# Kernel tuning notes

Hardware: AMD Instinct MI355X
Metric: run time of the kernel (lower is better)

Reference implementation:

```python
import jax, jax.numpy as jnp
import numpy as np
from jax import lax

B, N_SITES, FEAT, BOND, OUT = 2048, 128, 64, 32, 256
CORE_SCALE = 0.02  # keeps the 128-step matrix product finite


def setup_inputs() -> dict:
    key = jax.random.key(0)
    ks = jax.random.split(key, 6)
    return {
        "x": jax.random.normal(ks[0], (B, N_SITES, FEAT), dtype=jnp.float32),
        "cores": jax.random.normal(ks[1], (N_SITES, BOND, FEAT, BOND), dtype=jnp.float32) * CORE_SCALE,
        "start": jax.random.normal(ks[2], (1, BOND), dtype=jnp.float32),
        "end": jax.random.normal(ks[3], (BOND, 1), dtype=jnp.float32),
        "fc_w": jax.random.normal(ks[4], (OUT, 1), dtype=jnp.float32),
        "fc_b": jax.random.normal(ks[5], (OUT,), dtype=jnp.float32),
    }


def reference(x, cores, start, end, fc_w, fc_b):
    # x: [B, N, F]; cores: [N, D, F, D]; start: [1, D]; end: [D, 1]
    b = x.shape[0]
    res0 = jnp.broadcast_to(start, (b, start.shape[1]))  # [B, D]

    def step(res, site):
        xi, core = site  # xi: [B, F], core: [D, F, D]
        m = jnp.einsum('bf,dfr->bdr', xi, core)  # per-site transfer matrix [B, D, D]
        return jnp.einsum('bd,bdr->br', res, m), None

    res, _ = lax.scan(step, res0, (jnp.swapaxes(x, 0, 1), cores))
    val = res @ end  # [B, 1]
    return val @ fc_w.T + fc_b  # [B, OUT]
```

## Files before the change

kernel.cpp:

```cpp
#include <hip/hip_runtime.h>


#define NSITES 128
#define FEATD  64
#define BOND   32
#define OUTD   256
#define BT     16
#define SEGLEN 16
#define NSEG   (NSITES / SEGLEN)
#define NPAIR  (SEGLEN / 2)
#define NBT    (2048 / BT)

#define RSTRIDE 36
#define BSTRIDE 1164

typedef __attribute__((ext_vector_type(4))) float float4v;

__device__ __forceinline__ unsigned pk4_fp8(float a, float b, float c, float d) {
    int v = __builtin_amdgcn_cvt_pk_fp8_f32(a, b, 0, false);
    v = __builtin_amdgcn_cvt_pk_fp8_f32(c, d, v, true);
    return (unsigned)v;
}

__device__ __forceinline__ long ld8(const unsigned char* p) {
    unsigned lo = *(const unsigned*)p;
    unsigned hi = *(const unsigned*)(p + 4);
    return (long)(((unsigned long long)hi << 32) | (unsigned long long)lo);
}

__device__ __forceinline__ void af_load(long af[16], const unsigned char* __restrict__ core8,
                                        int n, int wave, int cl, int q) {
    const unsigned char* base = core8 + (size_t)n * (1024 * FEATD);
#pragma unroll
    for (int i = 0; i < 8; ++i) {
        const unsigned char* p = base + (size_t)((wave * 8 + i) * 16 + cl) * FEATD + q * 8;
        af[2 * i + 0] = *(const long*)p;
        af[2 * i + 1] = *(const long*)(p + 32);
    }
}

__device__ __forceinline__ long cvt_frag(float4v c0, float4v c1,
                                         int idxlo, int idxhi, int selhi) {
    const float s = 0.0625f;
    int d0 = (int)pk4_fp8(c0[0] * s, c0[1] * s, c0[2] * s, c0[3] * s);
    int d1 = (int)pk4_fp8(c1[0] * s, c1[1] * s, c1[2] * s, c1[3] * s);
    int l0 = __builtin_amdgcn_ds_bpermute(idxlo, d0);
    int l1 = __builtin_amdgcn_ds_bpermute(idxlo, d1);
    int h0 = __builtin_amdgcn_ds_bpermute(idxhi, d0);
    int h1 = __builtin_amdgcn_ds_bpermute(idxhi, d1);
    unsigned lo = (unsigned)(selhi ? l1 : l0);
    unsigned hi = (unsigned)(selhi ? h1 : h0);
    return (long)(((unsigned long long)hi << 32) | (unsigned long long)lo);
}

__global__ __launch_bounds__(256)
void prep_cores8(const float* __restrict__ cores, unsigned char* __restrict__ core8) {
    __shared__ float tile[FEATD][BOND + 4];
    const int nd = blockIdx.x;
    const int t  = threadIdx.x;
    const float* src = cores + (size_t)nd * (FEATD * BOND);
    {
        int base = t * 8;
        int f = base >> 5, r0 = base & 31;
        float4 v0 = *(const float4*)(src + base);
        float4 v1 = *(const float4*)(src + base + 4);
        tile[f][r0 + 0] = v0.x; tile[f][r0 + 1] = v0.y;
        tile[f][r0 + 2] = v0.z; tile[f][r0 + 3] = v0.w;
        tile[f][r0 + 4] = v1.x; tile[f][r0 + 5] = v1.y;
        tile[f][r0 + 6] = v1.z; tile[f][r0 + 7] = v1.w;
    }
    __syncthreads();
    const int r = t >> 3, f0 = (t & 7) * 8;
    const float s = 16.0f;
    unsigned lo = pk4_fp8(tile[f0 + 0][r] * s, tile[f0 + 1][r] * s,
                          tile[f0 + 2][r] * s, tile[f0 + 3][r] * s);
    unsigned hi = pk4_fp8(tile[f0 + 4][r] * s, tile[f0 + 5][r] * s,
                          tile[f0 + 6][r] * s, tile[f0 + 7][r] * s);
    uint2 w; w.x = lo; w.y = hi;
    *(uint2*)(core8 + ((size_t)nd * BOND + r) * FEATD + f0) = w;
}

__global__ __launch_bounds__(512, 4)
void mps_seg(const float* __restrict__ x, const unsigned char* __restrict__ core8,
             unsigned char* __restrict__ Pout) {
    __shared__ __align__(16) unsigned char MA[BT * BSTRIDE];
    __shared__ __align__(16) unsigned char MB[BT * BSTRIDE];
    __shared__ __align__(16) unsigned char XS[2][2][BT * 72];

    const int t    = threadIdx.x;
    const int wave = t >> 6;
    const int lane = t & 63;
    const int cl   = lane & 15;
    const int q    = lane >> 4;
    const int seg  = blockIdx.x;
    const int bt   = blockIdx.y;
    const int b0   = bt * BT;
    const int xb   = t >> 5, xf = (t & 31) * 2;

    const int idxlo = (cl + 16 * ((2 * q) & 3)) << 2;
    const int idxhi = (cl + 16 * ((2 * q + 1) & 3)) << 2;
    const int selhi = q >> 1;

    long ps[2][2];
#pragma unroll
    for (int J = 0; J < 2; ++J) {
        int row = J * 16 + cl;
        int jj  = row - 8 * q;
        long v  = (jj >= 0 && jj < 8) ? (long)(0x58ULL << (8 * jj)) : 0L;
        ps[0][J] = v;
        ps[1][J] = v;
    }

    const int n0 = seg * SEGLEN;

    const float* xptr = x + ((size_t)(b0 + xb) * NSITES + n0) * FEATD + xf;
    float2 xa  = *(const float2*)xptr;
    float2 xbv = *(const float2*)(xptr + FEATD);
    {
        int v0 = __builtin_amdgcn_cvt_pk_fp8_f32(xa.x, xa.y, 0, false);
        *(unsigned short*)&XS[0][0][xb * 72 + xf] = (unsigned short)(v0 & 0xffff);
        int v1 = __builtin_amdgcn_cvt_pk_fp8_f32(xbv.x, xbv.y, 0, false);
        *(unsigned short*)&XS[0][1][xb * 72 + xf] = (unsigned short)(v1 & 0xffff);
    }
    long afa[16];
    af_load(afa, core8, n0, wave, cl, q);
    __syncthreads();

    for (int j = 0; j < NPAIR; ++j) {
        const int n = n0 + 2 * j;

        {
            const unsigned char* xsA = &XS[j & 1][0][0];
            const unsigned char* xsB = &XS[j & 1][1][0];
            long bxa0 = *(const long*)(xsA + cl * 72 + q * 8);
            long bxa1 = *(const long*)(xsA + cl * 72 + 32 + q * 8);
            long bxb0 = *(const long*)(xsB + cl * 72 + q * 8);
            long bxb1 = *(const long*)(xsB + cl * 72 + 32 + q * 8);

            long afb[16];
            af_load(afb, core8, n + 1, wave, cl, q);

            float4v acc[8];
            __builtin_amdgcn_s_setprio(1);
#pragma unroll
            for (int i = 0; i < 8; ++i) {
                float4v z = {0.f, 0.f, 0.f, 0.f};
                z = __builtin_amdgcn_mfma_f32_16x16x32_fp8_fp8(afa[2 * i + 0], bxa0, z, 0, 0, 0);
                acc[i] = __builtin_amdgcn_mfma_f32_16x16x32_fp8_fp8(afa[2 * i + 1], bxa1, z, 0, 0, 0);
            }
            __builtin_amdgcn_s_setprio(0);
#pragma unroll
            for (int i = 0; i < 8; ++i) {
                unsigned w = pk4_fp8(acc[i][0], acc[i][1], acc[i][2], acc[i][3]);
                *(unsigned*)&MA[cl * BSTRIDE + (wave * 4 + (i >> 1)) * RSTRIDE
                                + (i & 1) * 16 + q * 4] = w;
            }

            if (j + 1 < NPAIR) {
                const float* xp = x + ((size_t)(b0 + xb) * NSITES + n + 2) * FEATD + xf;
                xa  = *(const float2*)xp;
                xbv = *(const float2*)(xp + FEATD);
            }

            float4v accb[8];
            __builtin_amdgcn_s_setprio(1);
#pragma unroll
            for (int i = 0; i < 8; ++i) {
                float4v z = {0.f, 0.f, 0.f, 0.f};
                z = __builtin_amdgcn_mfma_f32_16x16x32_fp8_fp8(afb[2 * i + 0], bxb0, z, 0, 0, 0);
                accb[i] = __builtin_amdgcn_mfma_f32_16x16x32_fp8_fp8(afb[2 * i + 1], bxb1, z, 0, 0, 0);
            }
            __builtin_amdgcn_s_setprio(0);
#pragma unroll
            for (int p = 0; p < 2; ++p)
#pragma unroll
                for (int g = 0; g < 4; ++g) {
                    unsigned w = pk4_fp8(accb[0 + p][g], accb[2 + p][g],
                                         accb[4 + p][g], accb[6 + p][g]);
                    *(unsigned*)&MB[cl * BSTRIDE + (16 * p + 4 * q + g) * RSTRIDE
                                    + wave * 4] = w;
                }
        }
        __syncthreads();

        {
            if (j + 1 < NPAIR) {
                int v0 = __builtin_amdgcn_cvt_pk_fp8_f32(xa.x, xa.y, 0, false);
                *(unsigned short*)&XS[(j + 1) & 1][0][xb * 72 + xf] = (unsigned short)(v0 & 0xffff);
                int v1 = __builtin_amdgcn_cvt_pk_fp8_f32(xbv.x, xbv.y, 0, false);
                *(unsigned short*)&XS[(j + 1) & 1][1][xb * 72 + xf] = (unsigned short)(v1 & 0xffff);
                af_load(afa, core8, n + 2, wave, cl, q);
            }

#pragma unroll
            for (int bi = 0; bi < 2; ++bi) {
                const int bb = wave * 2 + bi;
                const unsigned char* mab = &MA[bb * BSTRIDE];
                const unsigned char* mbb = &MB[bb * BSTRIDE];
                long pa0 = ld8(mab + cl * RSTRIDE + q * 8);
                long pa1 = ld8(mab + (16 + cl) * RSTRIDE + q * 8);
                long pb0 = ld8(mbb + cl * RSTRIDE + q * 8);
                long pb1 = ld8(mbb + (16 + cl) * RSTRIDE + q * 8);
                float4v z00 = {0.f, 0.f, 0.f, 0.f}, z01 = {0.f, 0.f, 0.f, 0.f};
                float4v z10 = {0.f, 0.f, 0.f, 0.f}, z11 = {0.f, 0.f, 0.f, 0.f};
                z00 = __builtin_amdgcn_mfma_f32_16x16x32_fp8_fp8(pa0, pb0, z00, 0, 0, 0);
                z01 = __builtin_amdgcn_mfma_f32_16x16x32_fp8_fp8(pa0, pb1, z01, 0, 0, 0);
                z10 = __builtin_amdgcn_mfma_f32_16x16x32_fp8_fp8(pa1, pb0, z10, 0, 0, 0);
                z11 = __builtin_amdgcn_mfma_f32_16x16x32_fp8_fp8(pa1, pb1, z11, 0, 0, 0);
                long ca0 = cvt_frag(z00, z10, idxlo, idxhi, selhi);
                long ca1 = cvt_frag(z01, z11, idxlo, idxhi, selhi);
                float4v c00 = {0.f, 0.f, 0.f, 0.f}, c01 = {0.f, 0.f, 0.f, 0.f};
                float4v c10 = {0.f, 0.f, 0.f, 0.f}, c11 = {0.f, 0.f, 0.f, 0.f};
                c00 = __builtin_amdgcn_mfma_f32_16x16x32_fp8_fp8(ca0, ps[bi][0], c00, 0, 0, 0);
                c01 = __builtin_amdgcn_mfma_f32_16x16x32_fp8_fp8(ca0, ps[bi][1], c01, 0, 0, 0);
                c10 = __builtin_amdgcn_mfma_f32_16x16x32_fp8_fp8(ca1, ps[bi][0], c10, 0, 0, 0);
                c11 = __builtin_amdgcn_mfma_f32_16x16x32_fp8_fp8(ca1, ps[bi][1], c11, 0, 0, 0);
                ps[bi][0] = cvt_frag(c00, c10, idxlo, idxhi, selhi);
                ps[bi][1] = cvt_frag(c01, c11, idxlo, idxhi, selhi);
            }
        }
        __syncthreads();
    }

#pragma unroll
    for (int bi = 0; bi < 2; ++bi) {
        const int bb = wave * 2 + bi;
#pragma unroll
        for (int J = 0; J < 2; ++J)
            *(long*)&MA[bb * 1024 + (J * 16 + cl) * 32 + q * 8] = ps[bi][J];
    }
    __syncthreads();
    {
        const uint4* p = (const uint4*)&MA[t * 32];
        uint4* g = (uint4*)(Pout + ((size_t)seg * 2048 + b0) * 1024 + (size_t)t * 32);
        g[0] = p[0];
        g[1] = p[1];
    }
}

__global__ __launch_bounds__(256)
void combine(const unsigned char* __restrict__ Pout, const float* __restrict__ startv,
             const float* __restrict__ endv, const float* __restrict__ fc_w,
             const float* __restrict__ fc_b, float* __restrict__ out) {
    __shared__ __align__(16) unsigned char st[8 * 1024];
    __shared__ float resA[8][33], resB[8][33];
    __shared__ float val[8];
    const int t  = threadIdx.x;
    const int b0 = blockIdx.x * 8;
    const int bb = t >> 5, r = t & 31;

    uint4 ga[NSEG][2];
#pragma unroll
    for (int s = 0; s < NSEG; ++s) {
        const uint4* g = (const uint4*)(Pout + ((size_t)s * 2048 + b0) * 1024 + (size_t)t * 32);
        ga[s][0] = g[0];
        ga[s][1] = g[1];
    }

    resA[bb][r] = startv[r];
    for (int s = 0; s < NSEG; ++s) {
        {
            uint4* p = (uint4*)&st[t * 32];
            p[0] = ga[s][0];
            p[1] = ga[s][1];
        }
        __syncthreads();
        const float* rin = (s & 1) ? &resB[bb][0] : &resA[bb][0];
        float* rout      = (s & 1) ? &resA[bb][0] : &resB[bb][0];
        float acc = 0.f;
#pragma unroll
        for (int d = 0; d < BOND; ++d) {
            int byte = st[bb * 1024 + d * 32 + r];
            acc += rin[d] * __builtin_amdgcn_cvt_f32_fp8(byte, 0);
        }
        rout[r] = acc * 0.0625f;
        __syncthreads();
    }
    float prod = resA[bb][r] * endv[r];
#pragma unroll
    for (int off = 16; off >= 1; off >>= 1) prod += __shfl_down(prod, off, 32);
    if (r == 0) val[bb] = prod;
    __syncthreads();

    const float v = val[t >> 5];
    const int j0 = (t & 31) * 8;
    const int ob = b0 + (t >> 5);
#pragma unroll
    for (int i = 0; i < 2; ++i) {
        int j = j0 + i * 4;
        float4 w4 = *(const float4*)(fc_w + j);
        float4 bbv = *(const float4*)(fc_b + j);
        float4 o;
        o.x = v * w4.x + bbv.x;
        o.y = v * w4.y + bbv.y;
        o.z = v * w4.z + bbv.z;
        o.w = v * w4.w + bbv.w;
        *(float4*)(out + (size_t)ob * OUTD + j) = o;
    }
}

extern "C" void kernel_launch(void* const* d_in, const int* in_sizes, int n_in,
                              void* d_out, int out_size, void* d_ws, size_t ws_size,
                              hipStream_t stream) {
    const float* x      = (const float*)d_in[0];
    const float* cores  = (const float*)d_in[1];
    const float* startv = (const float*)d_in[2];
    const float* endv   = (const float*)d_in[3];
    const float* fc_w   = (const float*)d_in[4];
    const float* fc_b   = (const float*)d_in[5];
    float* out = (float*)d_out;

    unsigned char* core8 = (unsigned char*)d_ws;
    unsigned char* Pout  = core8 + (size_t)NSITES * 1024 * FEATD;

    prep_cores8<<<NSITES * BOND, 256, 0, stream>>>(cores, core8);
    mps_seg<<<dim3(NSEG, NBT), 512, 0, stream>>>(x, core8, Pout);
    combine<<<2048 / 8, 256, 0, stream>>>(Pout, startv, endv, fc_w, fc_b, out);
}
```

Before: 253.1 us.

## Double-buffer transfer-matrix tiles to overlap build and chain phases

The MA/MB shared buffers are double-buffered so the next pair's transfer matrices are built while the current pair is chained into the running product. This cuts the two barriers per site pair down to one and lets the build MFMAs interleave with the dependent chain MFMAs. The cost is doubled LDS for the matrix buffers, which may reduce occupancy against the launch bound of 4 blocks. It also drops the s_setprio hints and adds a prologue and epilogue.

```diff
diff --git a/kernel.cpp b/kernel.cpp
--- a/kernel.cpp
+++ b/kernel.cpp
@@ -13,6 +13,7 @@
 
 #define RSTRIDE 36
 #define BSTRIDE 1164
+#define MSIZE   (BT * BSTRIDE)
 
 typedef __attribute__((ext_vector_type(4))) float float4v;
 
@@ -53,6 +54,46 @@
     return (long)(((unsigned long long)hi << 32) | (unsigned long long)lo);
 }
 
+__device__ __forceinline__ void build_a(const long af[16], const unsigned char* xs,
+                                        unsigned char* MA, int wave, int cl, int q) {
+    long bx0 = *(const long*)(xs + cl * 72 + q * 8);
+    long bx1 = *(const long*)(xs + cl * 72 + 32 + q * 8);
+    float4v acc[8];
+#pragma unroll
+    for (int i = 0; i < 8; ++i) {
+        float4v z = {0.f, 0.f, 0.f, 0.f};
+        z = __builtin_amdgcn_mfma_f32_16x16x32_fp8_fp8(af[2 * i + 0], bx0, z, 0, 0, 0);
+        acc[i] = __builtin_amdgcn_mfma_f32_16x16x32_fp8_fp8(af[2 * i + 1], bx1, z, 0, 0, 0);
+    }
+#pragma unroll
+    for (int i = 0; i < 8; ++i) {
+        unsigned w = pk4_fp8(acc[i][0], acc[i][1], acc[i][2], acc[i][3]);
+        *(unsigned*)&MA[cl * BSTRIDE + (wave * 4 + (i >> 1)) * RSTRIDE
+                        + (i & 1) * 16 + q * 4] = w;
+    }
+}
+
+__device__ __forceinline__ void build_b(const long af[16], const unsigned char* xs,
+                                        unsigned char* MB, int wave, int cl, int q) {
+    long bx0 = *(const long*)(xs + cl * 72 + q * 8);
+    long bx1 = *(const long*)(xs + cl * 72 + 32 + q * 8);
+    float4v acc[8];
+#pragma unroll
+    for (int i = 0; i < 8; ++i) {
+        float4v z = {0.f, 0.f, 0.f, 0.f};
+        z = __builtin_amdgcn_mfma_f32_16x16x32_fp8_fp8(af[2 * i + 0], bx0, z, 0, 0, 0);
+        acc[i] = __builtin_amdgcn_mfma_f32_16x16x32_fp8_fp8(af[2 * i + 1], bx1, z, 0, 0, 0);
+    }
+#pragma unroll
+    for (int p = 0; p < 2; ++p)
+#pragma unroll
+        for (int g = 0; g < 4; ++g) {
+            unsigned w = pk4_fp8(acc[0 + p][g], acc[2 + p][g],
+                                 acc[4 + p][g], acc[6 + p][g]);
+            *(unsigned*)&MB[cl * BSTRIDE + (16 * p + 4 * q + g) * RSTRIDE + wave * 4] = w;
+        }
+}
+
 __global__ __launch_bounds__(256)
 void prep_cores8(const float* __restrict__ cores, unsigned char* __restrict__ core8) {
     __shared__ float tile[FEATD][BOND + 4];
@@ -83,8 +124,7 @@
 __global__ __launch_bounds__(512, 4)
 void mps_seg(const float* __restrict__ x, const unsigned char* __restrict__ core8,
              unsigned char* __restrict__ Pout) {
-    __shared__ __align__(16) unsigned char MA[BT * BSTRIDE];
-    __shared__ __align__(16) unsigned char MB[BT * BSTRIDE];
+    __shared__ __align__(16) unsigned char BUF[2][2 * MSIZE];
     __shared__ __align__(16) unsigned char XS[2][2][BT * 72];
 
     const int t    = threadIdx.x;
@@ -112,114 +152,125 @@
     }
 
     const int n0 = seg * SEGLEN;
-
-    const float* xptr = x + ((size_t)(b0 + xb) * NSITES + n0) * FEATD + xf;
-    float2 xa  = *(const float2*)xptr;
-    float2 xbv = *(const float2*)(xptr + FEATD);
-    {
-        int v0 = __builtin_amdgcn_cvt_pk_fp8_f32(xa.x, xa.y, 0, false);
+    const float* xbase = x + (size_t)(b0 + xb) * NSITES * FEATD + xf;
+
+    {
+        float2 a = *(const float2*)(xbase + (size_t)(n0 + 0) * FEATD);
+        float2 b = *(const float2*)(xbase + (size_t)(n0 + 1) * FEATD);
+        int v0 = __builtin_amdgcn_cvt_pk_fp8_f32(a.x, a.y, 0, false);
         *(unsigned short*)&XS[0][0][xb * 72 + xf] = (unsigned short)(v0 & 0xffff);
-        int v1 = __builtin_amdgcn_cvt_pk_fp8_f32(xbv.x, xbv.y, 0, false);
+        int v1 = __builtin_amdgcn_cvt_pk_fp8_f32(b.x, b.y, 0, false);
         *(unsigned short*)&XS[0][1][xb * 72 + xf] = (unsigned short)(v1 & 0xffff);
     }
     long afa[16];
     af_load(afa, core8, n0, wave, cl, q);
-    __syncthreads();
-
-    for (int j = 0; j < NPAIR; ++j) {
-        const int n = n0 + 2 * j;
+    float2 xa  = *(const float2*)(xbase + (size_t)(n0 + 2) * FEATD);
+    float2 xbv = *(const float2*)(xbase + (size_t)(n0 + 3) * FEATD);
+    __syncthreads();
+
+    {
+        long afb[16];
+        af_load(afb, core8, n0 + 1, wave, cl, q);
+        build_a(afa, &XS[0][0][0], BUF[0], wave, cl, q);
+        build_b(afb, &XS[0][1][0], BUF[0] + MSIZE, wave, cl, q);
+    }
+    {
+        int v0 = __builtin_amdgcn_cvt_pk_fp8_f32(xa.x, xa.y, 0, false);
+        *(unsigned short*)&XS[1][0][xb * 72 + xf] = (unsigned short)(v0 & 0xffff);
+        int v1 = __builtin_amdgcn_cvt_pk_fp8_f32(xbv.x, xbv.y, 0, false);
+        *(unsigned short*)&XS[1][1][xb * 72 + xf] = (unsigned short)(v1 & 0xffff);
+    }
+    af_load(afa, core8, n0 + 2, wave, cl, q);
+    xa  = *(const float2*)(xbase + (size_t)(n0 + 4) * FEATD);
+    xbv = *(const float2*)(xbase + (size_t)(n0 + 5) * FEATD);
+    __syncthreads();
+
+    for (int j = 0; j < NPAIR - 1; ++j) {
+        const int jn = j + 1;
+        const unsigned char* MAc = BUF[j & 1];
+        const unsigned char* MBc = BUF[j & 1] + MSIZE;
+        unsigned char* MAn = BUF[jn & 1];
+        unsigned char* MBn = BUF[jn & 1] + MSIZE;
+
+        long pa[2][2], pb[2][2];
+#pragma unroll
+        for (int bi = 0; bi < 2; ++bi) {
+            const int bb = wave * 2 + bi;
+            pa[bi][0] = ld8(MAc + bb * BSTRIDE + cl * RSTRIDE + q * 8);
+            pa[bi][1] = ld8(MAc + bb * BSTRIDE + (16 + cl) * RSTRIDE + q * 8);
+            pb[bi][0] = ld8(MBc + bb * BSTRIDE + cl * RSTRIDE + q * 8);
+            pb[bi][1] = ld8(MBc + bb * BSTRIDE + (16 + cl) * RSTRIDE + q * 8);
+        }
 
         {
-            const unsigned char* xsA = &XS[j & 1][0][0];
-            const unsigned char* xsB = &XS[j & 1][1][0];
-            long bxa0 = *(const long*)(xsA + cl * 72 + q * 8);
-            long bxa1 = *(const long*)(xsA + cl * 72 + 32 + q * 8);
-            long bxb0 = *(const long*)(xsB + cl * 72 + q * 8);
-            long bxb1 = *(const long*)(xsB + cl * 72 + 32 + q * 8);
-
             long afb[16];
-            af_load(afb, core8, n + 1, wave, cl, q);
-
-            float4v acc[8];
-            __builtin_amdgcn_s_setprio(1);
-#pragma unroll
-            for (int i = 0; i < 8; ++i) {
-                float4v z = {0.f, 0.f, 0.f, 0.f};
-                z = __builtin_amdgcn_mfma_f32_16x16x32_fp8_fp8(afa[2 * i + 0], bxa0, z, 0, 0, 0);
-                acc[i] = __builtin_amdgcn_mfma_f32_16x16x32_fp8_fp8(afa[2 * i + 1], bxa1, z, 0, 0, 0);
+            af_load(afb, core8, n0 + 2 * jn + 1, wave, cl, q);
+            build_a(afa, &XS[jn & 1][0][0], MAn, wave, cl, q);
+            build_b(afb, &XS[jn & 1][1][0], MBn, wave, cl, q);
+        }
+
+        if (j + 2 < NPAIR) {
+            int v0 = __builtin_amdgcn_cvt_pk_fp8_f32(xa.x, xa.y, 0, false);
+            *(unsigned short*)&XS[(j + 2) & 1][0][xb * 72 + xf] = (unsigned short)(v0 & 0xffff);
+            int v1 = __builtin_amdgcn_cvt_pk_fp8_f32(xbv.x, xbv.y, 0, false);
+            *(unsigned short*)&XS[(j + 2) & 1][1][xb * 72 + xf] = (unsigned short)(v1 & 0xffff);
+            af_load(afa, core8, n0 + 2 * (j + 2), wave, cl, q);
+            if (j + 3 < NPAIR) {
+                xa  = *(const float2*)(xbase + (size_t)(n0 + 2 * (j + 3)) * FEATD);
+                xbv = *(const float2*)(xbase + (size_t)(n0 + 2 * (j + 3) + 1) * FEATD);
             }
-            __builtin_amdgcn_s_setprio(0);
-#pragma unroll
-            for (int i = 0; i < 8; ++i) {
-                unsigned w = pk4_fp8(acc[i][0], acc[i][1], acc[i][2], acc[i][3]);
-                *(unsigned*)&MA[cl * BSTRIDE + (wave * 4 + (i >> 1)) * RSTRIDE
-                                + (i & 1) * 16 + q * 4] = w;
-            }
-
-            if (j + 1 < NPAIR) {
-                const float* xp = x + ((size_t)(b0 + xb) * NSITES + n + 2) * FEATD + xf;
-                xa  = *(const float2*)xp;
-                xbv = *(const float2*)(xp + FEATD);
-            }
-
-            float4v accb[8];
-            __builtin_amdgcn_s_setprio(1);
-#pragma unroll
-            for (int i = 0; i < 8; ++i) {
-                float4v z = {0.f, 0.f, 0.f, 0.f};
-                z = __builtin_amdgcn_mfma_f32_16x16x32_fp8_fp8(afb[2 * i + 0], bxb0, z, 0, 0, 0);
-                accb[i] = __builtin_amdgcn_mfma_f32_16x16x32_fp8_fp8(afb[2 * i + 1], bxb1, z, 0, 0, 0);
-            }
-            __builtin_amdgcn_s_setprio(0);
-#pragma unroll
-            for (int p = 0; p < 2; ++p)
-#pragma unroll
-                for (int g = 0; g < 4; ++g) {
-                    unsigned w = pk4_fp8(accb[0 + p][g], accb[2 + p][g],
-                                         accb[4 + p][g], accb[6 + p][g]);
-                    *(unsigned*)&MB[cl * BSTRIDE + (16 * p + 4 * q + g) * RSTRIDE
-                                    + wave * 4] = w;
-                }
-        }
+        }
+
+#pragma unroll
+        for (int bi = 0; bi < 2; ++bi) {
+            float4v z00 = {0.f, 0.f, 0.f, 0.f}, z01 = {0.f, 0.f, 0.f, 0.f};
+            float4v z10 = {0.f, 0.f, 0.f, 0.f}, z11 = {0.f, 0.f, 0.f, 0.f};
+            z00 = __builtin_amdgcn_mfma_f32_16x16x32_fp8_fp8(pa[bi][0], pb[bi][0], z00, 0, 0, 0);
+            z01 = __builtin_amdgcn_mfma_f32_16x16x32_fp8_fp8(pa[bi][0], pb[bi][1], z01, 0, 0, 0);
+            z10 = __builtin_amdgcn_mfma_f32_16x16x32_fp8_fp8(pa[bi][1], pb[bi][0], z10, 0, 0, 0);
+            z11 = __builtin_amdgcn_mfma_f32_16x16x32_fp8_fp8(pa[bi][1], pb[bi][1], z11, 0, 0, 0);
+            long ca0 = cvt_frag(z00, z10, idxlo, idxhi, selhi);
+            long ca1 = cvt_frag(z01, z11, idxlo, idxhi, selhi);
+            float4v c00 = {0.f, 0.f, 0.f, 0.f}, c01 = {0.f, 0.f, 0.f, 0.f};
+            float4v c10 = {0.f, 0.f, 0.f, 0.f}, c11 = {0.f, 0.f, 0.f, 0.f};
+            c00 = __builtin_amdgcn_mfma_f32_16x16x32_fp8_fp8(ca0, ps[bi][0], c00, 0, 0, 0);
+            c01 = __builtin_amdgcn_mfma_f32_16x16x32_fp8_fp8(ca0, ps[bi][1], c01, 0, 0, 0);
+            c10 = __builtin_amdgcn_mfma_f32_16x16x32_fp8_fp8(ca1, ps[bi][0], c10, 0, 0, 0);
+            c11 = __builtin_amdgcn_mfma_f32_16x16x32_fp8_fp8(ca1, ps[bi][1], c11, 0, 0, 0);
+            ps[bi][0] = cvt_frag(c00, c10, idxlo, idxhi, selhi);
+            ps[bi][1] = cvt_frag(c01, c11, idxlo, idxhi, selhi);
+        }
+
         __syncthreads();
-
-        {
-            if (j + 1 < NPAIR) {
-                int v0 = __builtin_amdgcn_cvt_pk_fp8_f32(xa.x, xa.y, 0, false);
-                *(unsigned short*)&XS[(j + 1) & 1][0][xb * 72 + xf] = (unsigned short)(v0 & 0xffff);
-                int v1 = __builtin_amdgcn_cvt_pk_fp8_f32(xbv.x, xbv.y, 0, false);
-                *(unsigned short*)&XS[(j + 1) & 1][1][xb * 72 + xf] = (unsigned short)(v1 & 0xffff);
-                af_load(afa, core8, n + 2, wave, cl, q);
-            }
-
-#pragma unroll
-            for (int bi = 0; bi < 2; ++bi) {
-                const int bb = wave * 2 + bi;
-                const unsigned char* mab = &MA[bb * BSTRIDE];
-                const unsigned char* mbb = &MB[bb * BSTRIDE];
-                long pa0 = ld8(mab + cl * RSTRIDE + q * 8);
-                long pa1 = ld8(mab + (16 + cl) * RSTRIDE + q * 8);
-                long pb0 = ld8(mbb + cl * RSTRIDE + q * 8);
-                long pb1 = ld8(mbb + (16 + cl) * RSTRIDE + q * 8);
-                float4v z00 = {0.f, 0.f, 0.f, 0.f}, z01 = {0.f, 0.f, 0.f, 0.f};
-                float4v z10 = {0.f, 0.f, 0.f, 0.f}, z11 = {0.f, 0.f, 0.f, 0.f};
-                z00 = __builtin_amdgcn_mfma_f32_16x16x32_fp8_fp8(pa0, pb0, z00, 0, 0, 0);
-                z01 = __builtin_amdgcn_mfma_f32_16x16x32_fp8_fp8(pa0, pb1, z01, 0, 0, 0);
-                z10 = __builtin_amdgcn_mfma_f32_16x16x32_fp8_fp8(pa1, pb0, z10, 0, 0, 0);
-                z11 = __builtin_amdgcn_mfma_f32_16x16x32_fp8_fp8(pa1, pb1, z11, 0, 0, 0);
-                long ca0 = cvt_frag(z00, z10, idxlo, idxhi, selhi);
-                long ca1 = cvt_frag(z01, z11, idxlo, idxhi, selhi);
-                float4v c00 = {0.f, 0.f, 0.f, 0.f}, c01 = {0.f, 0.f, 0.f, 0.f};
-                float4v c10 = {0.f, 0.f, 0.f, 0.f}, c11 = {0.f, 0.f, 0.f, 0.f};
-                c00 = __builtin_amdgcn_mfma_f32_16x16x32_fp8_fp8(ca0, ps[bi][0], c00, 0, 0, 0);
-                c01 = __builtin_amdgcn_mfma_f32_16x16x32_fp8_fp8(ca0, ps[bi][1], c01, 0, 0, 0);
-                c10 = __builtin_amdgcn_mfma_f32_16x16x32_fp8_fp8(ca1, ps[bi][0], c10, 0, 0, 0);
-                c11 = __builtin_amdgcn_mfma_f32_16x16x32_fp8_fp8(ca1, ps[bi][1], c11, 0, 0, 0);
-                ps[bi][0] = cvt_frag(c00, c10, idxlo, idxhi, selhi);
-                ps[bi][1] = cvt_frag(c01, c11, idxlo, idxhi, selhi);
-            }
-        }
-        __syncthreads();
+    }
+
+    {
+        const unsigned char* MAc = BUF[(NPAIR - 1) & 1];
+        const unsigned char* MBc = BUF[(NPAIR - 1) & 1] + MSIZE;
+#pragma unroll
+        for (int bi = 0; bi < 2; ++bi) {
+            const int bb = wave * 2 + bi;
+            long pa0 = ld8(MAc + bb * BSTRIDE + cl * RSTRIDE + q * 8);
+            long pa1 = ld8(MAc + bb * BSTRIDE + (16 + cl) * RSTRIDE + q * 8);
+            long pb0 = ld8(MBc + bb * BSTRIDE + cl * RSTRIDE + q * 8);
+            long pb1 = ld8(MBc + bb * BSTRIDE + (16 + cl) * RSTRIDE + q * 8);
+            float4v z00 = {0.f, 0.f, 0.f, 0.f}, z01 = {0.f, 0.f, 0.f, 0.f};
+            float4v z10 = {0.f, 0.f, 0.f, 0.f}, z11 = {0.f, 0.f, 0.f, 0.f};
+            z00 = __builtin_amdgcn_mfma_f32_16x16x32_fp8_fp8(pa0, pb0, z00, 0, 0, 0);
+            z01 = __builtin_amdgcn_mfma_f32_16x16x32_fp8_fp8(pa0, pb1, z01, 0, 0, 0);
+            z10 = __builtin_amdgcn_mfma_f32_16x16x32_fp8_fp8(pa1, pb0, z10, 0, 0, 0);
+            z11 = __builtin_amdgcn_mfma_f32_16x16x32_fp8_fp8(pa1, pb1, z11, 0, 0, 0);
+            long ca0 = cvt_frag(z00, z10, idxlo, idxhi, selhi);
+            long ca1 = cvt_frag(z01, z11, idxlo, idxhi, selhi);
+            float4v c00 = {0.f, 0.f, 0.f, 0.f}, c01 = {0.f, 0.f, 0.f, 0.f};
+            float4v c10 = {0.f, 0.f, 0.f, 0.f}, c11 = {0.f, 0.f, 0.f, 0.f};
+            c00 = __builtin_amdgcn_mfma_f32_16x16x32_fp8_fp8(ca0, ps[bi][0], c00, 0, 0, 0);
+            c01 = __builtin_amdgcn_mfma_f32_16x16x32_fp8_fp8(ca0, ps[bi][1], c01, 0, 0, 0);
+            c10 = __builtin_amdgcn_mfma_f32_16x16x32_fp8_fp8(ca1, ps[bi][0], c10, 0, 0, 0);
+            c11 = __builtin_amdgcn_mfma_f32_16x16x32_fp8_fp8(ca1, ps[bi][1], c11, 0, 0, 0);
+            ps[bi][0] = cvt_frag(c00, c10, idxlo, idxhi, selhi);
+            ps[bi][1] = cvt_frag(c01, c11, idxlo, idxhi, selhi);
+        }
     }
 
 #pragma unroll
@@ -227,11 +278,11 @@
         const int bb = wave * 2 + bi;
 #pragma unroll
         for (int J = 0; J < 2; ++J)
-            *(long*)&MA[bb * 1024 + (J * 16 + cl) * 32 + q * 8] = ps[bi][J];
-    }
-    __syncthreads();
-    {
-        const uint4* p = (const uint4*)&MA[t * 32];
+            *(long*)&BUF[0][bb * 1024 + (J * 16 + cl) * 32 + q * 8] = ps[bi][J];
+    }
+    __syncthreads();
+    {
+        const uint4* p = (const uint4*)&BUF[0][t * 32];
         uint4* g = (uint4*)(Pout + ((size_t)seg * 2048 + b0) * 1024 + (size_t)t * 32);
         g[0] = p[0];
         g[1] = p[1];
```

Result: slower. 259.5 us (+2.6%).

## Software-pipeline MPS segment kernel with double-buffered swizzled LDS and one barrier

Applied to the files above, without the earlier changes.

The loop is restructured so that building the next pair of fp8 transfer matrices overlaps with the chained matrix products of the current pair. A double-buffered LDS area with XOR-swizzled addressing allows one __syncthreads per iteration instead of two. x is now loaded and converted to fp8 directly in registers, replacing the XS staging in shared memory, and the last pair's chain is peeled into an epilogue. The intent is to remove barrier stalls and LDS bank conflicts. The risk is that LDS per block grows to 64KB, which may limit occupancy, and that register pressure rises.

```diff
diff --git a/kernel.cpp b/kernel.cpp
--- a/kernel.cpp
+++ b/kernel.cpp
@@ -11,8 +11,8 @@
 #define NPAIR  (SEGLEN / 2)
 #define NBT    (2048 / BT)
 
-#define RSTRIDE 36
-#define BSTRIDE 1164
+#define MAHALF 16384
+#define BUFSZ  32768
 
 typedef __attribute__((ext_vector_type(4))) float float4v;
 
@@ -20,23 +20,6 @@
     int v = __builtin_amdgcn_cvt_pk_fp8_f32(a, b, 0, false);
     v = __builtin_amdgcn_cvt_pk_fp8_f32(c, d, v, true);
     return (unsigned)v;
-}
-
-__device__ __forceinline__ long ld8(const unsigned char* p) {
-    unsigned lo = *(const unsigned*)p;
-    unsigned hi = *(const unsigned*)(p + 4);
-    return (long)(((unsigned long long)hi << 32) | (unsigned long long)lo);
-}
-
-__device__ __forceinline__ void af_load(long af[16], const unsigned char* __restrict__ core8,
-                                        int n, int wave, int cl, int q) {
-    const unsigned char* base = core8 + (size_t)n * (1024 * FEATD);
-#pragma unroll
-    for (int i = 0; i < 8; ++i) {
-        const unsigned char* p = base + (size_t)((wave * 8 + i) * 16 + cl) * FEATD + q * 8;
-        af[2 * i + 0] = *(const long*)p;
-        af[2 * i + 1] = *(const long*)(p + 32);
-    }
 }
 
 __device__ __forceinline__ long cvt_frag(float4v c0, float4v c1,
@@ -51,6 +34,49 @@
     unsigned lo = (unsigned)(selhi ? l1 : l0);
     unsigned hi = (unsigned)(selhi ? h1 : h0);
     return (long)(((unsigned long long)hi << 32) | (unsigned long long)lo);
+}
+
+__device__ __forceinline__ void build_mfmas(const long af[16], long bx0, long bx1,
+                                            float4v acc[8]) {
+#pragma unroll
+    for (int i = 0; i < 8; ++i) {
+        float4v z = {0.f, 0.f, 0.f, 0.f};
+        z = __builtin_amdgcn_mfma_f32_16x16x32_fp8_fp8(af[2 * i + 0], bx0, z, 0, 0, 0);
+        acc[i] = __builtin_amdgcn_mfma_f32_16x16x32_fp8_fp8(af[2 * i + 1], bx1, z, 0, 0, 0);
+    }
+}
+
+__device__ __forceinline__ void packA(const float4v acc[8], unsigned char* buf, int vA) {
+#pragma unroll
+    for (int i = 0; i < 8; ++i)
+        *(unsigned*)&buf[vA + i * 128] =
+            pk4_fp8(acc[i][0], acc[i][1], acc[i][2], acc[i][3]);
+}
+
+__device__ __forceinline__ void packB(const float4v acc[8], unsigned char* buf, int vB) {
+#pragma unroll
+    for (int p = 0; p < 2; ++p)
+#pragma unroll
+        for (int g = 0; g < 4; ++g)
+            *(unsigned*)&buf[vB + g * 256 + p * 128] =
+                pk4_fp8(acc[0 + p][g], acc[2 + p][g], acc[4 + p][g], acc[6 + p][g]);
+}
+
+__device__ __forceinline__ void xload(const float* xlane, int s, float4 r[4]) {
+    const float* p = xlane + (size_t)s * FEATD;
+    r[0] = *(const float4*)(p);
+    r[1] = *(const float4*)(p + 4);
+    r[2] = *(const float4*)(p + 32);
+    r[3] = *(const float4*)(p + 36);
+}
+
+__device__ __forceinline__ void xcvt(const float4 r[4], long& b0, long& b1) {
+    unsigned l0 = pk4_fp8(r[0].x, r[0].y, r[0].z, r[0].w);
+    unsigned h0 = pk4_fp8(r[1].x, r[1].y, r[1].z, r[1].w);
+    unsigned l1 = pk4_fp8(r[2].x, r[2].y, r[2].z, r[2].w);
+    unsigned h1 = pk4_fp8(r[3].x, r[3].y, r[3].z, r[3].w);
+    b0 = (long)(((unsigned long long)h0 << 32) | l0);
+    b1 = (long)(((unsigned long long)h1 << 32) | l1);
 }
 
 __global__ __launch_bounds__(256)
@@ -83,9 +109,7 @@
 __global__ __launch_bounds__(512, 4)
 void mps_seg(const float* __restrict__ x, const unsigned char* __restrict__ core8,
              unsigned char* __restrict__ Pout) {
-    __shared__ __align__(16) unsigned char MA[BT * BSTRIDE];
-    __shared__ __align__(16) unsigned char MB[BT * BSTRIDE];
-    __shared__ __align__(16) unsigned char XS[2][2][BT * 72];
+    __shared__ __align__(16) unsigned char BUF[2][BUFSZ];
 
     const int t    = threadIdx.x;
     const int wave = t >> 6;
@@ -95,7 +119,25 @@
     const int seg  = blockIdx.x;
     const int bt   = blockIdx.y;
     const int b0   = bt * BT;
-    const int xb   = t >> 5, xf = (t & 31) * 2;
+
+    const int vA = (cl << 10)
+                 + (((((q >> 1) & 1) | ((wave & 3) << 1)) ^ (cl & 7)) << 4)
+                 + (((wave >> 2) & 1) << 3) + ((q & 1) << 2);
+    const int vB = MAHALF + (cl << 10)
+                 + ((((q & 3) | (((wave >> 1) & 3) << 2)) ^ (cl & 15)) << 3)
+                 + ((wave & 1) << 2);
+
+    const int permA = (q & 1) | (((cl >> 2) & 1) << 1) | (((cl >> 3) & 1) << 2)
+                    | (((q >> 1) & 1) << 3) | ((cl & 1) << 4) | (((cl >> 1) & 1) << 5);
+    const int sB0 = ((cl >> 2) & 3) | ((q & 3) << 2) | ((cl & 3) << 5);
+    int aA[2], aB0[2], aB1[2];
+#pragma unroll
+    for (int bi = 0; bi < 2; ++bi) {
+        int bb = wave * 2 + bi;
+        aA[bi]  = (bb << 10) + ((permA ^ (bb & 7)) << 4);
+        aB0[bi] = MAHALF + (bb << 10) + ((sB0 ^ (bb & 15)) << 3);
+        aB1[bi] = MAHALF + (bb << 10) + (((sB0 | 16) ^ (bb & 15)) << 3);
+    }
 
     const int idxlo = (cl + 16 * ((2 * q) & 3)) << 2;
     const int idxhi = (cl + 16 * ((2 * q + 1) & 3)) << 2;
@@ -112,114 +154,120 @@
     }
 
     const int n0 = seg * SEGLEN;
-
-    const float* xptr = x + ((size_t)(b0 + xb) * NSITES + n0) * FEATD + xf;
-    float2 xa  = *(const float2*)xptr;
-    float2 xbv = *(const float2*)(xptr + FEATD);
+    const float* xlane = x + ((size_t)(b0 + cl) * NSITES + n0) * FEATD + q * 8;
+    const unsigned char* cbase = core8 + (size_t)n0 * (1024 * FEATD)
+                               + (size_t)(wave * 8192 + cl * 64 + q * 8);
+#define AF_LOAD(A, s_) { const unsigned char* p_ = cbase + (size_t)(s_) * 65536; \
+    _Pragma("unroll") for (int i_ = 0; i_ < 8; ++i_) { \
+        (A)[2*i_+0] = *(const long*)(p_ + i_*1024); \
+        (A)[2*i_+1] = *(const long*)(p_ + i_*1024 + 32); } }
+
+    long af[16];
+    long bxe0, bxe1, bxo0, bxo1;
+    float4 ra[4], rb[4];
+
+    AF_LOAD(af, 0);
+    xload(xlane, 0, ra);
+    xload(xlane, 1, rb);
+    xcvt(ra, bxe0, bxe1);
+    xcvt(rb, bxo0, bxo1);
     {
-        int v0 = __builtin_amdgcn_cvt_pk_fp8_f32(xa.x, xa.y, 0, false);
-        *(unsigned short*)&XS[0][0][xb * 72 + xf] = (unsigned short)(v0 & 0xffff);
-        int v1 = __builtin_amdgcn_cvt_pk_fp8_f32(xbv.x, xbv.y, 0, false);
-        *(unsigned short*)&XS[0][1][xb * 72 + xf] = (unsigned short)(v1 & 0xffff);
-    }
-    long afa[16];
-    af_load(afa, core8, n0, wave, cl, q);
+        float4v acc[8];
+        build_mfmas(af, bxe0, bxe1, acc);
+        AF_LOAD(af, 1);
+        packA(acc, BUF[0], vA);
+        xload(xlane, 2, ra);
+        float4v accb[8];
+        build_mfmas(af, bxo0, bxo1, accb);
+        AF_LOAD(af, 2);
+        packB(accb, BUF[0], vB);
+        xload(xlane, 3, rb);
+    }
     __syncthreads();
 
-    for (int j = 0; j < NPAIR; ++j) {
-        const int n = n0 + 2 * j;
+    for (int j = 0; j < NPAIR - 1; ++j) {
+        const unsigned char* bufc = BUF[j & 1];
+        unsigned char* bufn = BUF[(j + 1) & 1];
+
+        xcvt(ra, bxe0, bxe1);
+        xcvt(rb, bxo0, bxo1);
+
+        long pa0[2], pa1[2], pb0[2], pb1[2];
+#pragma unroll
+        for (int bi = 0; bi < 2; ++bi) {
+            uint4 v = *(const uint4*)(bufc + aA[bi]);
+            pa0[bi] = (long)(((unsigned long long)v.y << 32) | v.x);
+            pa1[bi] = (long)(((unsigned long long)v.w << 32) | v.z);
+            pb0[bi] = *(const long*)(bufc + aB0[bi]);
+            pb1[bi] = *(const long*)(bufc + aB1[bi]);
+        }
 
         {
-            const unsigned char* xsA = &XS[j & 1][0][0];
-            const unsigned char* xsB = &XS[j & 1][1][0];
-            long bxa0 = *(const long*)(xsA + cl * 72 + q * 8);
-            long bxa1 = *(const long*)(xsA + cl * 72 + 32 + q * 8);
-            long bxb0 = *(const long*)(xsB + cl * 72 + q * 8);
-            long bxb1 = *(const long*)(xsB + cl * 72 + 32 + q * 8);
-
-            long afb[16];
-            af_load(afb, core8, n + 1, wave, cl, q);
-
             float4v acc[8];
-            __builtin_amdgcn_s_setprio(1);
-#pragma unroll
-            for (int i = 0; i < 8; ++i) {
-                float4v z = {0.f, 0.f, 0.f, 0.f};
-                z = __builtin_amdgcn_mfma_f32_16x16x32_fp8_fp8(afa[2 * i + 0], bxa0, z, 0, 0, 0);
-                acc[i] = __builtin_amdgcn_mfma_f32_16x16x32_fp8_fp8(afa[2 * i + 1], bxa1, z, 0, 0, 0);
-            }
-            __builtin_amdgcn_s_setprio(0);
-#pragma unroll
-            for (int i = 0; i < 8; ++i) {
-                unsigned w = pk4_fp8(acc[i][0], acc[i][1], acc[i][2], acc[i][3]);
-                *(unsigned*)&MA[cl * BSTRIDE + (wave * 4 + (i >> 1)) * RSTRIDE
-                                + (i & 1) * 16 + q * 4] = w;
-            }
-
-            if (j + 1 < NPAIR) {
-                const float* xp = x + ((size_t)(b0 + xb) * NSITES + n + 2) * FEATD + xf;
-                xa  = *(const float2*)xp;
-                xbv = *(const float2*)(xp + FEATD);
-            }
-
+            build_mfmas(af, bxe0, bxe1, acc);
+            AF_LOAD(af, 2 * j + 3);
+            packA(acc, bufn, vA);
+        }
+        const bool more = (j + 2 < NPAIR);
+        xload(xlane, more ? 2 * j + 4 : 0, ra);
+        {
             float4v accb[8];
-            __builtin_amdgcn_s_setprio(1);
-#pragma unroll
-            for (int i = 0; i < 8; ++i) {
-                float4v z = {0.f, 0.f, 0.f, 0.f};
-                z = __builtin_amdgcn_mfma_f32_16x16x32_fp8_fp8(afb[2 * i + 0], bxb0, z, 0, 0, 0);
-                accb[i] = __builtin_amdgcn_mfma_f32_16x16x32_fp8_fp8(afb[2 * i + 1], bxb1, z, 0, 0, 0);
-            }
-            __builtin_amdgcn_s_setprio(0);
-#pragma unroll
-            for (int p = 0; p < 2; ++p)
-#pragma unroll
-                for (int g = 0; g < 4; ++g) {
-                    unsigned w = pk4_fp8(accb[0 + p][g], accb[2 + p][g],
-                                         accb[4 + p][g], accb[6 + p][g]);
-                    *(unsigned*)&MB[cl * BSTRIDE + (16 * p + 4 * q + g) * RSTRIDE
-                                    + wave * 4] = w;
-                }
-        }
+            build_mfmas(af, bxo0, bxo1, accb);
+            AF_LOAD(af, (j + 1 < NPAIR - 1) ? 2 * j + 4 : 0);
+            packB(accb, bufn, vB);
+        }
+        xload(xlane, more ? 2 * j + 5 : 0, rb);
+
+        __builtin_amdgcn_s_setprio(1);
+#pragma unroll
+        for (int bi = 0; bi < 2; ++bi) {
+            float4v z00 = {0.f,0.f,0.f,0.f}, z01 = {0.f,0.f,0.f,0.f};
+            float4v z10 = {0.f,0.f,0.f,0.f}, z11 = {0.f,0.f,0.f,0.f};
+            z00 = __builtin_amdgcn_mfma_f32_16x16x32_fp8_fp8(pa0[bi], pb0[bi], z00, 0, 0, 0);
+            z01 = __builtin_amdgcn_mfma_f32_16x16x32_fp8_fp8(pa0[bi], pb1[bi], z01, 0, 0, 0);
+            z10 = __builtin_amdgcn_mfma_f32_16x16x32_fp8_fp8(pa1[bi], pb0[bi], z10, 0, 0, 0);
+            z11 = __builtin_amdgcn_mfma_f32_16x16x32_fp8_fp8(pa1[bi], pb1[bi], z11, 0, 0, 0);
+            long ca0 = cvt_frag(z00, z10, idxlo, idxhi, selhi);
+            long ca1 = cvt_frag(z01, z11, idxlo, idxhi, selhi);
+            float4v c00 = {0.f,0.f,0.f,0.f}, c01 = {0.f,0.f,0.f,0.f};
+            float4v c10 = {0.f,0.f,0.f,0.f}, c11 = {0.f,0.f,0.f,0.f};
+            c00 = __builtin_amdgcn_mfma_f32_16x16x32_fp8_fp8(ca0, ps[bi][0], c00, 0, 0, 0);
+            c01 = __builtin_amdgcn_mfma_f32_16x16x32_fp8_fp8(ca0, ps[bi][1], c01, 0, 0, 0);
+            c10 = __builtin_amdgcn_mfma_f32_16x16x32_fp8_fp8(ca1, ps[bi][0], c10, 0, 0, 0);
+            c11 = __builtin_amdgcn_mfma_f32_16x16x32_fp8_fp8(ca1, ps[bi][1], c11, 0, 0, 0);
+            ps[bi][0] = cvt_frag(c00, c10, idxlo, idxhi, selhi);
+            ps[bi][1] = cvt_frag(c01, c11, idxlo, idxhi, selhi);
+        }
+        __builtin_amdgcn_s_setprio(0);
         __syncthreads();
-
-        {
-            if (j + 1 < NPAIR) {
-                int v0 = __builtin_amdgcn_cvt_pk_fp8_f32(xa.x, xa.y, 0, false);
-                *(unsigned short*)&XS[(j + 1) & 1][0][xb * 72 + xf] = (unsigned short)(v0 & 0xffff);
-                int v1 = __builtin_amdgcn_cvt_pk_fp8_f32(xbv.x, xbv.y, 0, false);
-                *(unsigned short*)&XS[(j + 1) & 1][1][xb * 72 + xf] = (unsigned short)(v1 & 0xffff);
-                af_load(afa, core8, n + 2, wave, cl, q);
-            }
-
-#pragma unroll
-            for (int bi = 0; bi < 2; ++bi) {
-                const int bb = wave * 2 + bi;
-                const unsigned char* mab = &MA[bb * BSTRIDE];
-                const unsigned char* mbb = &MB[bb * BSTRIDE];
-                long pa0 = ld8(mab + cl * RSTRIDE + q * 8);
-                long pa1 = ld8(mab + (16 + cl) * RSTRIDE + q * 8);
-                long pb0 = ld8(mbb + cl * RSTRIDE + q * 8);
-                long pb1 = ld8(mbb + (16 + cl) * RSTRIDE + q * 8);
-                float4v z00 = {0.f, 0.f, 0.f, 0.f}, z01 = {0.f, 0.f, 0.f, 0.f};
-                float4v z10 = {0.f, 0.f, 0.f, 0.f}, z11 = {0.f, 0.f, 0.f, 0.f};
-                z00 = __builtin_amdgcn_mfma_f32_16x16x32_fp8_fp8(pa0, pb0, z00, 0, 0, 0);
-                z01 = __builtin_amdgcn_mfma_f32_16x16x32_fp8_fp8(pa0, pb1, z01, 0, 0, 0);
-                z10 = __builtin_amdgcn_mfma_f32_16x16x32_fp8_fp8(pa1, pb0, z10, 0, 0, 0);
-                z11 = __builtin_amdgcn_mfma_f32_16x16x32_fp8_fp8(pa1, pb1, z11, 0, 0, 0);
-                long ca0 = cvt_frag(z00, z10, idxlo, idxhi, selhi);
-                long ca1 = cvt_frag(z01, z11, idxlo, idxhi, selhi);
-                float4v c00 = {0.f, 0.f, 0.f, 0.f}, c01 = {0.f, 0.f, 0.f, 0.f};
-                float4v c10 = {0.f, 0.f, 0.f, 0.f}, c11 = {0.f, 0.f, 0.f, 0.f};
-                c00 = __builtin_amdgcn_mfma_f32_16x16x32_fp8_fp8(ca0, ps[bi][0], c00, 0, 0, 0);
-                c01 = __builtin_amdgcn_mfma_f32_16x16x32_fp8_fp8(ca0, ps[bi][1], c01, 0, 0, 0);
-                c10 = __builtin_amdgcn_mfma_f32_16x16x32_fp8_fp8(ca1, ps[bi][0], c10, 0, 0, 0);
-                c11 = __builtin_amdgcn_mfma_f32_16x16x32_fp8_fp8(ca1, ps[bi][1], c11, 0, 0, 0);
-                ps[bi][0] = cvt_frag(c00, c10, idxlo, idxhi, selhi);
-                ps[bi][1] = cvt_frag(c01, c11, idxlo, idxhi, selhi);
-            }
-        }
-        __syncthreads();
+    }
+
+    {
+        const unsigned char* bufc = BUF[(NPAIR - 1) & 1];
+#pragma unroll
+        for (int bi = 0; bi < 2; ++bi) {
+            uint4 v = *(const uint4*)(bufc + aA[bi]);
+            long pa0 = (long)(((unsigned long long)v.y << 32) | v.x);
+            long pa1 = (long)(((unsigned long long)v.w << 32) | v.z);
+            long pb0 = *(const long*)(bufc + aB0[bi]);
+            long pb1 = *(const long*)(bufc + aB1[bi]);
+            float4v z00 = {0.f,0.f,0.f,0.f}, z01 = {0.f,0.f,0.f,0.f};
+            float4v z10 = {0.f,0.f,0.f,0.f}, z11 = {0.f,0.f,0.f,0.f};
+            z00 = __builtin_amdgcn_mfma_f32_16x16x32_fp8_fp8(pa0, pb0, z00, 0, 0, 0);
+            z01 = __builtin_amdgcn_mfma_f32_16x16x32_fp8_fp8(pa0, pb1, z01, 0, 0, 0);
+            z10 = __builtin_amdgcn_mfma_f32_16x16x32_fp8_fp8(pa1, pb0, z10, 0, 0, 0);
+            z11 = __builtin_amdgcn_mfma_f32_16x16x32_fp8_fp8(pa1, pb1, z11, 0, 0, 0);
+            long ca0 = cvt_frag(z00, z10, idxlo, idxhi, selhi);
+            long ca1 = cvt_frag(z01, z11, idxlo, idxhi, selhi);
+            float4v c00 = {0.f,0.f,0.f,0.f}, c01 = {0.f,0.f,0.f,0.f};
+            float4v c10 = {0.f,0.f,0.f,0.f}, c11 = {0.f,0.f,0.f,0.f};
+            c00 = __builtin_amdgcn_mfma_f32_16x16x32_fp8_fp8(ca0, ps[bi][0], c00, 0, 0, 0);
+            c01 = __builtin_amdgcn_mfma_f32_16x16x32_fp8_fp8(ca0, ps[bi][1], c01, 0, 0, 0);
+            c10 = __builtin_amdgcn_mfma_f32_16x16x32_fp8_fp8(ca1, ps[bi][0], c10, 0, 0, 0);
+            c11 = __builtin_amdgcn_mfma_f32_16x16x32_fp8_fp8(ca1, ps[bi][1], c11, 0, 0, 0);
+            ps[bi][0] = cvt_frag(c00, c10, idxlo, idxhi, selhi);
+            ps[bi][1] = cvt_frag(c01, c11, idxlo, idxhi, selhi);
+        }
     }
 
 #pragma unroll
@@ -227,15 +275,16 @@
         const int bb = wave * 2 + bi;
 #pragma unroll
         for (int J = 0; J < 2; ++J)
-            *(long*)&MA[bb * 1024 + (J * 16 + cl) * 32 + q * 8] = ps[bi][J];
+            *(long*)&BUF[0][bb * 1024 + (J * 16 + cl) * 32 + q * 8] = ps[bi][J];
     }
     __syncthreads();
     {
-        const uint4* p = (const uint4*)&MA[t * 32];
+        const uint4* p = (const uint4*)&BUF[0][t * 32];
         uint4* g = (uint4*)(Pout + ((size_t)seg * 2048 + b0) * 1024 + (size_t)t * 32);
         g[0] = p[0];
         g[1] = p[1];
     }
+#undef AF_LOAD
 }
 
 __global__ __launch_bounds__(256)
```

New measurement: 342.4 us. 35.3% more time.
